# Kernel tuning notes

Measured on AMD Instinct MI355X. Metric: run time of the kernel, lower is better.

The kernel has to match this reference:

```python
import jax, jax.numpy as jnp
import numpy as np

N_NODES = 100000
N_EDGES = 1250000
D_IN = 32
H = 64
EPS = 1e-5


def layer_norm(x, g, b):
    mu = jnp.mean(x, axis=-1, keepdims=True)
    var = jnp.mean(jnp.square(x - mu), axis=-1, keepdims=True)
    return (x - mu) * jax.lax.rsqrt(var + EPS) * g + b


def setup_inputs() -> dict:
    key = jax.random.key(0)
    ks = jax.random.split(key, 6)
    x = jax.random.normal(ks[0], (N_NODES, D_IN), dtype=jnp.float32)
    edge_index = jax.random.randint(ks[1], (2, N_EDGES), 0, N_NODES, dtype=jnp.int64)
    W1 = jax.random.normal(ks[2], (D_IN, H), dtype=jnp.float32) * (1.0 / np.sqrt(D_IN))
    b1 = jax.random.normal(ks[3], (H,), dtype=jnp.float32) * 0.01
    W2 = jax.random.normal(ks[4], (H, H), dtype=jnp.float32) * (1.0 / np.sqrt(H))
    b2 = jax.random.normal(ks[5], (H,), dtype=jnp.float32) * 0.01
    g1 = jnp.ones((H,), dtype=jnp.float32)
    beta1 = jnp.zeros((H,), dtype=jnp.float32)
    g2 = jnp.ones((H,), dtype=jnp.float32)
    beta2 = jnp.zeros((H,), dtype=jnp.float32)
    return {"x": x, "edge_index": edge_index, "W1": W1, "b1": b1, "g1": g1,
            "beta1": beta1, "W2": W2, "b2": b2, "g2": g2, "beta2": beta2}


def reference(x, edge_index, W1, b1, g1, beta1, W2, b2, g2, beta2):
    # node MLP: Linear -> LN -> ReLU, twice
    h = jax.nn.relu(layer_norm(x @ W1 + b1, g1, beta1))
    h = jax.nn.relu(layer_norm(h @ W2 + b2, g2, beta2))
    # message passing: gather source features, scatter-add to destinations
    row, col = edge_index[0], edge_index[1]
    aggr = jax.ops.segment_sum(h[col], row, num_segments=N_NODES)  # [N, H]
    return h + aggr
```

## Files before the change

### kernel.cpp

```cpp
#include <hip/hip_runtime.h>

#define N_NODES 100000
#define D_IN 32
#define H 64
#define EPS 1e-5f
#define RSTR 32
#define CAP 32
#define OV_CAP 32768

typedef float floatx2 __attribute__((ext_vector_type(2)));

__device__ __forceinline__ unsigned short f2bf(float f) {
    union { float f; unsigned int u; } c; c.f = f;
    unsigned int b = c.u + 0x7FFFu + ((c.u >> 16) & 1u);
    return (unsigned short)(b >> 16);
}
__device__ __forceinline__ float bf2f(unsigned short s) {
    union { unsigned int u; float f; } c; c.u = ((unsigned int)s) << 16;
    return c.f;
}

__global__ __launch_bounds__(256, 2) void fused_kernel(
    const float* __restrict__ x,
    const float* __restrict__ W1, const float* __restrict__ b1,
    const float* __restrict__ g1, const float* __restrict__ be1,
    const float* __restrict__ W2, const float* __restrict__ b2,
    const float* __restrict__ g2, const float* __restrict__ be2,
    unsigned short* __restrict__ hb, unsigned char* __restrict__ hb8,
    const int* __restrict__ ei, int* __restrict__ cnt, int* __restrict__ bkt,
    int* __restrict__ ovCnt, int2* __restrict__ ov,
    int E, int SB, int TOT)
{
    const int i = blockIdx.x;
    const int before = (int)((long long)i * SB / TOT);
    const int after  = (int)((long long)(i + 1) * SB / TOT);

    if (after > before) {
        int t = before * 256 + threadIdx.x;
        int e0 = t * 8;
        if (e0 >= E) return;

        int rows[8], cols[8], pos[8];
        if (e0 + 7 < E) {
            int4 r0 = *(const int4*)(ei + e0);
            int4 r1 = *(const int4*)(ei + e0 + 4);
            int4 c0 = *(const int4*)(ei + E + e0);
            int4 c1 = *(const int4*)(ei + E + e0 + 4);
            rows[0]=r0.x; rows[1]=r0.y; rows[2]=r0.z; rows[3]=r0.w;
            rows[4]=r1.x; rows[5]=r1.y; rows[6]=r1.z; rows[7]=r1.w;
            cols[0]=c0.x; cols[1]=c0.y; cols[2]=c0.z; cols[3]=c0.w;
            cols[4]=c1.x; cols[5]=c1.y; cols[6]=c1.z; cols[7]=c1.w;
        } else {
#pragma unroll
            for (int j = 0; j < 8; ++j) {
                int e = e0 + j;
                if (e < E) { rows[j] = ei[e]; cols[j] = ei[E + e]; }
                else rows[j] = -1;
            }
        }
#pragma unroll
        for (int j = 0; j < 8; ++j)
            if (rows[j] >= 0) pos[j] = atomicAdd(&cnt[rows[j]], 1);
#pragma unroll
        for (int j = 0; j < 8; ++j) {
            if (rows[j] < 0) continue;
            if (pos[j] < CAP) {
                __builtin_nontemporal_store(cols[j], &bkt[rows[j] * RSTR + pos[j]]);
            } else {
                int s = atomicAdd(ovCnt, 1);
                if (s < OV_CAP) ov[s] = make_int2(rows[j], cols[j]);
            }
        }
        return;
    }

    int gid = (i - before) * 256 + threadIdx.x;
    int node = gid < N_NODES ? gid : N_NODES - 1;

    float xr[D_IN];
    {
        const float4* xp = (const float4*)(x + (long long)node * D_IN);
#pragma unroll
        for (int i2 = 0; i2 < D_IN / 4; ++i2) {
            float4 v = xp[i2];
            xr[4*i2+0] = v.x; xr[4*i2+1] = v.y; xr[4*i2+2] = v.z; xr[4*i2+3] = v.w;
        }
    }

    float h1[H];
#pragma unroll
    for (int jb = 0; jb < H / 4; ++jb) {
        float4 b = *(const float4*)(b1 + jb * 4);
        h1[4*jb+0] = b.x; h1[4*jb+1] = b.y; h1[4*jb+2] = b.z; h1[4*jb+3] = b.w;
    }
#pragma unroll
    for (int k = 0; k < D_IN; ++k) {
        float xk = xr[k];
#pragma unroll
        for (int jb = 0; jb < H / 4; ++jb) {
            float4 w = *(const float4*)(W1 + k * H + jb * 4);
            h1[4*jb+0] += xk * w.x; h1[4*jb+1] += xk * w.y;
            h1[4*jb+2] += xk * w.z; h1[4*jb+3] += xk * w.w;
        }
    }
    {
        float s0=0,s1=0,s2=0,s3=0, q0=0,q1=0,q2=0,q3=0;
#pragma unroll
        for (int j = 0; j < H; j += 4) {
            s0 += h1[j+0]; s1 += h1[j+1]; s2 += h1[j+2]; s3 += h1[j+3];
            q0 += h1[j+0]*h1[j+0]; q1 += h1[j+1]*h1[j+1];
            q2 += h1[j+2]*h1[j+2]; q3 += h1[j+3]*h1[j+3];
        }
        float mu  = (s0+s1+s2+s3) * (1.0f / H);
        float var = (q0+q1+q2+q3) * (1.0f / H) - mu * mu;
        float rs  = rsqrtf(var + EPS);
#pragma unroll
        for (int jb = 0; jb < H / 4; ++jb) {
            float4 g = *(const float4*)(g1 + jb * 4);
            float4 be = *(const float4*)(be1 + jb * 4);
            h1[4*jb+0] = fmaxf((h1[4*jb+0]-mu)*rs*g.x + be.x, 0.0f);
            h1[4*jb+1] = fmaxf((h1[4*jb+1]-mu)*rs*g.y + be.y, 0.0f);
            h1[4*jb+2] = fmaxf((h1[4*jb+2]-mu)*rs*g.z + be.z, 0.0f);
            h1[4*jb+3] = fmaxf((h1[4*jb+3]-mu)*rs*g.w + be.w, 0.0f);
        }
    }

    float h2[H];
#pragma unroll
    for (int jb = 0; jb < H / 4; ++jb) {
        float4 b = *(const float4*)(b2 + jb * 4);
        h2[4*jb+0] = b.x; h2[4*jb+1] = b.y; h2[4*jb+2] = b.z; h2[4*jb+3] = b.w;
    }
#pragma unroll
    for (int k = 0; k < H; ++k) {
        float hk = h1[k];
#pragma unroll
        for (int jb = 0; jb < H / 4; ++jb) {
            float4 w = *(const float4*)(W2 + k * H + jb * 4);
            h2[4*jb+0] += hk * w.x; h2[4*jb+1] += hk * w.y;
            h2[4*jb+2] += hk * w.z; h2[4*jb+3] += hk * w.w;
        }
    }
    {
        float s0=0,s1=0,s2=0,s3=0, q0=0,q1=0,q2=0,q3=0;
#pragma unroll
        for (int j = 0; j < H; j += 4) {
            s0 += h2[j+0]; s1 += h2[j+1]; s2 += h2[j+2]; s3 += h2[j+3];
            q0 += h2[j+0]*h2[j+0]; q1 += h2[j+1]*h2[j+1];
            q2 += h2[j+2]*h2[j+2]; q3 += h2[j+3]*h2[j+3];
        }
        float mu  = (s0+s1+s2+s3) * (1.0f / H);
        float var = (q0+q1+q2+q3) * (1.0f / H) - mu * mu;
        float rs  = rsqrtf(var + EPS);

        unsigned short* hp = hb + (long long)node * H;
        unsigned int w8[H / 4];
#pragma unroll
        for (int jb = 0; jb < H / 4; ++jb) {
            float4 g = *(const float4*)(g2 + jb * 4);
            float4 be = *(const float4*)(be2 + jb * 4);
            float4 v;
            v.x = fmaxf((h2[4*jb+0]-mu)*rs*g.x + be.x, 0.0f);
            v.y = fmaxf((h2[4*jb+1]-mu)*rs*g.y + be.y, 0.0f);
            v.z = fmaxf((h2[4*jb+2]-mu)*rs*g.z + be.z, 0.0f);
            v.w = fmaxf((h2[4*jb+3]-mu)*rs*g.w + be.w, 0.0f);
            ushort4 u;
            u.x = f2bf(v.x); u.y = f2bf(v.y); u.z = f2bf(v.z); u.w = f2bf(v.w);
            *(ushort4*)(hp + 4*jb) = u;
            int lo = __builtin_amdgcn_cvt_pk_fp8_f32(v.x, v.y, 0, false);
            w8[jb] = (unsigned int)__builtin_amdgcn_cvt_pk_fp8_f32(v.z, v.w, lo, true);
        }
        unsigned int* hp8 = (unsigned int*)(hb8 + (long long)node * H);
#pragma unroll
        for (int q = 0; q < H / 16; ++q)
            *(uint4*)(hp8 + q * 4) = make_uint4(w8[4*q+0], w8[4*q+1], w8[4*q+2], w8[4*q+3]);
    }
}

__global__ __launch_bounds__(256, 2) void aggr_kernel(
    const int* __restrict__ cnt, const int* __restrict__ bkt,
    const unsigned short* __restrict__ hb, const unsigned char* __restrict__ hb8,
    float* __restrict__ out,
    const int* __restrict__ ovCnt, const int2* __restrict__ ov)
{
    const int t    = threadIdx.x & 63;
    const int sub  = t >> 4;
    const int c    = t & 15;
    const int wave = blockIdx.x * 4 + (threadIdx.x >> 6);
    const int node = wave * 4 + sub;

    int m = cnt[node];
    if (m > CAP) m = CAP;
    const int base = node * RSTR;
    const unsigned int* h8 = (const unsigned int*)hb8;

    float a0 = 0.f, a1 = 0.f, a2 = 0.f, a3 = 0.f;
#pragma unroll
    for (int j0 = 0; j0 < CAP; j0 += 16) {
        int cc[16];
#pragma unroll
        for (int i = 0; i < 16; ++i)
            cc[i] = bkt[base + j0 + i];
        unsigned int vv[16];
#pragma unroll
        for (int i = 0; i < 16; ++i)
            if (j0 + i < m) vv[i] = h8[(cc[i] << 4) + c];
#pragma unroll
        for (int i = 0; i < 16; ++i) {
            if (j0 + i < m) {
                floatx2 p0 = __builtin_amdgcn_cvt_pk_f32_fp8(vv[i], false);
                floatx2 p1 = __builtin_amdgcn_cvt_pk_f32_fp8(vv[i], true);
                a0 += p0.x; a1 += p0.y; a2 += p1.x; a3 += p1.y;
            }
        }
    }

    {
        uint2 sv = *(const uint2*)(hb + ((long long)node << 6) + (c << 2));
        a0 += bf2f((unsigned short)(sv.x & 0xFFFFu));
        a1 += bf2f((unsigned short)(sv.x >> 16));
        a2 += bf2f((unsigned short)(sv.y & 0xFFFFu));
        a3 += bf2f((unsigned short)(sv.y >> 16));
    }

    int nov = *ovCnt; if (nov > OV_CAP) nov = OV_CAP;
    for (int i = 0; i < nov; ++i) {
        int2 rc = ov[i];
        if (rc.x == node) {
            uint2 vv = *(const uint2*)(hb + ((long long)rc.y << 6) + (c << 2));
            a0 += bf2f((unsigned short)(vv.x & 0xFFFFu));
            a1 += bf2f((unsigned short)(vv.x >> 16));
            a2 += bf2f((unsigned short)(vv.y & 0xFFFFu));
            a3 += bf2f((unsigned short)(vv.y >> 16));
        }
    }

    *(float4*)(out + ((long long)node << 6) + (c << 2)) = make_float4(a0, a1, a2, a3);
}

extern "C" void kernel_launch(void* const* d_in, const int* in_sizes, int n_in,
                              void* d_out, int out_size, void* d_ws, size_t ws_size,
                              hipStream_t stream)
{
    const float* x   = (const float*)d_in[0];
    const int*   ei  = (const int*)d_in[1];
    const float* W1  = (const float*)d_in[2];
    const float* b1  = (const float*)d_in[3];
    const float* g1  = (const float*)d_in[4];
    const float* be1 = (const float*)d_in[5];
    const float* W2  = (const float*)d_in[6];
    const float* b2  = (const float*)d_in[7];
    const float* g2  = (const float*)d_in[8];
    const float* be2 = (const float*)d_in[9];

    float* out = (float*)d_out;

    char* ws = (char*)d_ws;
    unsigned short* hb    = (unsigned short*)ws;
    unsigned char*  hb8   = (unsigned char*)(ws + 12800000);
    int*            cnt   = (int*)(ws + 19200000);
    int*            ovCnt = (int*)(ws + 19600000);
    int2*           ov    = (int2*)(ws + 19600064);
    int*            bkt   = (int*)(ws + 19862208);

    const int E = in_sizes[1] / 2;

    hipMemsetAsync(cnt, 0, 400064, stream);

    const int SB = ((E + 7) / 8 + 255) / 256;
    const int MB = (N_NODES + 255) / 256;
    fused_kernel<<<SB + MB, 256, 0, stream>>>(
        x, W1, b1, g1, be1, W2, b2, g2, be2, hb, hb8,
        ei, cnt, bkt, ovCnt, ov, E, SB, SB + MB);

    aggr_kernel<<<N_NODES / 16, 256, 0, stream>>>(cnt, bkt, hb, hb8, out, ovCnt, ov);
}
```

Before: 209.7 us.

## Partition edge buckets by source-node half and aggregate in two passes

Edges are bucketed per destination node into two sub-buckets of 16 slots, split by whether the gathered source node is in the lower or upper half of the node range. Aggregation then runs as two kernel launches, each gathering only from one half of the fp8 feature table, so each pass's working set is smaller and more likely to stay in cache. The second pass does a read-modify-write of the output. Per-half capacity drops to 16, which may push more edges into the overflow list that is scanned linearly. It also adds an extra launch and doubles the counter array and memset.

```diff
diff --git a/kernel.cpp b/kernel.cpp
--- a/kernel.cpp
+++ b/kernel.cpp
@@ -5,7 +5,8 @@
 #define H 64
 #define EPS 1e-5f
 #define RSTR 32
-#define CAP 32
+#define SCAP 16
+#define HALF 50000
 #define OV_CAP 32768
 
 typedef float floatx2 __attribute__((ext_vector_type(2)));
@@ -27,7 +28,7 @@
     const float* __restrict__ W2, const float* __restrict__ b2,
     const float* __restrict__ g2, const float* __restrict__ be2,
     unsigned short* __restrict__ hb, unsigned char* __restrict__ hb8,
-    const int* __restrict__ ei, int* __restrict__ cnt, int* __restrict__ bkt,
+    const int* __restrict__ ei, int* __restrict__ cnt2, int* __restrict__ bkt,
     int* __restrict__ ovCnt, int2* __restrict__ ov,
     int E, int SB, int TOT)
 {
@@ -40,7 +41,7 @@
         int e0 = t * 8;
         if (e0 >= E) return;
 
-        int rows[8], cols[8], pos[8];
+        int rows[8], cols[8], pos[8], gg[8];
         if (e0 + 7 < E) {
             int4 r0 = *(const int4*)(ei + e0);
             int4 r1 = *(const int4*)(ei + e0 + 4);
@@ -59,13 +60,18 @@
             }
         }
 #pragma unroll
-        for (int j = 0; j < 8; ++j)
-            if (rows[j] >= 0) pos[j] = atomicAdd(&cnt[rows[j]], 1);
+        for (int j = 0; j < 8; ++j) {
+            if (rows[j] >= 0) {
+                gg[j] = (cols[j] >= HALF) ? 1 : 0;
+                pos[j] = atomicAdd(&cnt2[rows[j] * 2 + gg[j]], 1);
+            }
+        }
 #pragma unroll
         for (int j = 0; j < 8; ++j) {
             if (rows[j] < 0) continue;
-            if (pos[j] < CAP) {
-                __builtin_nontemporal_store(cols[j], &bkt[rows[j] * RSTR + pos[j]]);
+            if (pos[j] < SCAP) {
+                __builtin_nontemporal_store(cols[j],
+                    &bkt[rows[j] * RSTR + gg[j] * SCAP + pos[j]]);
             } else {
                 int s = atomicAdd(ovCnt, 1);
                 if (s < OV_CAP) ov[s] = make_int2(rows[j], cols[j]);
@@ -177,11 +183,11 @@
     }
 }
 
-__global__ __launch_bounds__(256, 2) void aggr_kernel(
-    const int* __restrict__ cnt, const int* __restrict__ bkt,
+__global__ __launch_bounds__(256) void aggr_kernel(
+    const int* __restrict__ cnt2, const int* __restrict__ bkt,
     const unsigned short* __restrict__ hb, const unsigned char* __restrict__ hb8,
     float* __restrict__ out,
-    const int* __restrict__ ovCnt, const int2* __restrict__ ov)
+    const int* __restrict__ ovCnt, const int2* __restrict__ ov, int g)
 {
     const int t    = threadIdx.x & 63;
     const int sub  = t >> 4;
@@ -189,53 +195,52 @@
     const int wave = blockIdx.x * 4 + (threadIdx.x >> 6);
     const int node = wave * 4 + sub;
 
-    int m = cnt[node];
-    if (m > CAP) m = CAP;
-    const int base = node * RSTR;
+    int m = cnt2[node * 2 + g];
+    if (m > SCAP) m = SCAP;
+    const int base = node * RSTR + g * SCAP;
     const unsigned int* h8 = (const unsigned int*)hb8;
 
     float a0 = 0.f, a1 = 0.f, a2 = 0.f, a3 = 0.f;
-#pragma unroll
-    for (int j0 = 0; j0 < CAP; j0 += 16) {
-        int cc[16];
-#pragma unroll
-        for (int i = 0; i < 16; ++i)
-            cc[i] = bkt[base + j0 + i];
-        unsigned int vv[16];
-#pragma unroll
-        for (int i = 0; i < 16; ++i)
-            if (j0 + i < m) vv[i] = h8[(cc[i] << 4) + c];
-#pragma unroll
-        for (int i = 0; i < 16; ++i) {
-            if (j0 + i < m) {
-                floatx2 p0 = __builtin_amdgcn_cvt_pk_f32_fp8(vv[i], false);
-                floatx2 p1 = __builtin_amdgcn_cvt_pk_f32_fp8(vv[i], true);
-                a0 += p0.x; a1 += p0.y; a2 += p1.x; a3 += p1.y;
-            }
-        }
-    }
-
-    {
+    int cc[SCAP];
+#pragma unroll
+    for (int i = 0; i < SCAP; ++i)
+        cc[i] = bkt[base + i];
+    unsigned int vv[SCAP];
+#pragma unroll
+    for (int i = 0; i < SCAP; ++i)
+        if (i < m) vv[i] = h8[(cc[i] << 4) + c];
+#pragma unroll
+    for (int i = 0; i < SCAP; ++i) {
+        if (i < m) {
+            floatx2 p0 = __builtin_amdgcn_cvt_pk_f32_fp8(vv[i], false);
+            floatx2 p1 = __builtin_amdgcn_cvt_pk_f32_fp8(vv[i], true);
+            a0 += p0.x; a1 += p0.y; a2 += p1.x; a3 += p1.y;
+        }
+    }
+
+    float* op = out + ((long long)node << 6) + (c << 2);
+    if (g == 0) {
         uint2 sv = *(const uint2*)(hb + ((long long)node << 6) + (c << 2));
         a0 += bf2f((unsigned short)(sv.x & 0xFFFFu));
         a1 += bf2f((unsigned short)(sv.x >> 16));
         a2 += bf2f((unsigned short)(sv.y & 0xFFFFu));
         a3 += bf2f((unsigned short)(sv.y >> 16));
-    }
-
-    int nov = *ovCnt; if (nov > OV_CAP) nov = OV_CAP;
-    for (int i = 0; i < nov; ++i) {
-        int2 rc = ov[i];
-        if (rc.x == node) {
-            uint2 vv = *(const uint2*)(hb + ((long long)rc.y << 6) + (c << 2));
-            a0 += bf2f((unsigned short)(vv.x & 0xFFFFu));
-            a1 += bf2f((unsigned short)(vv.x >> 16));
-            a2 += bf2f((unsigned short)(vv.y & 0xFFFFu));
-            a3 += bf2f((unsigned short)(vv.y >> 16));
-        }
-    }
-
-    *(float4*)(out + ((long long)node << 6) + (c << 2)) = make_float4(a0, a1, a2, a3);
+        *(float4*)op = make_float4(a0, a1, a2, a3);
+    } else {
+        int nov = *ovCnt; if (nov > OV_CAP) nov = OV_CAP;
+        for (int i = 0; i < nov; ++i) {
+            int2 rc = ov[i];
+            if (rc.x == node) {
+                uint2 vb = *(const uint2*)(hb + ((long long)rc.y << 6) + (c << 2));
+                a0 += bf2f((unsigned short)(vb.x & 0xFFFFu));
+                a1 += bf2f((unsigned short)(vb.x >> 16));
+                a2 += bf2f((unsigned short)(vb.y & 0xFFFFu));
+                a3 += bf2f((unsigned short)(vb.y >> 16));
+            }
+        }
+        float4 prev = *(float4*)op;
+        *(float4*)op = make_float4(prev.x + a0, prev.y + a1, prev.z + a2, prev.w + a3);
+    }
 }
 
 extern "C" void kernel_launch(void* const* d_in, const int* in_sizes, int n_in,
@@ -258,20 +263,21 @@
     char* ws = (char*)d_ws;
     unsigned short* hb    = (unsigned short*)ws;
     unsigned char*  hb8   = (unsigned char*)(ws + 12800000);
-    int*            cnt   = (int*)(ws + 19200000);
-    int*            ovCnt = (int*)(ws + 19600000);
-    int2*           ov    = (int2*)(ws + 19600064);
-    int*            bkt   = (int*)(ws + 19862208);
+    int*            cnt2  = (int*)(ws + 19200000);
+    int*            ovCnt = (int*)(ws + 20000000);
+    int2*           ov    = (int2*)(ws + 20000064);
+    int*            bkt   = (int*)(ws + 20262208);
 
     const int E = in_sizes[1] / 2;
 
-    hipMemsetAsync(cnt, 0, 400064, stream);
+    hipMemsetAsync(cnt2, 0, 800064, stream);
 
     const int SB = ((E + 7) / 8 + 255) / 256;
     const int MB = (N_NODES + 255) / 256;
     fused_kernel<<<SB + MB, 256, 0, stream>>>(
         x, W1, b1, g1, be1, W2, b2, g2, be2, hb, hb8,
-        ei, cnt, bkt, ovCnt, ov, E, SB, SB + MB);
-
-    aggr_kernel<<<N_NODES / 16, 256, 0, stream>>>(cnt, bkt, hb, hb8, out, ovCnt, ov);
-}
+        ei, cnt2, bkt, ovCnt, ov, E, SB, SB + MB);
+
+    aggr_kernel<<<N_NODES / 16, 256, 0, stream>>>(cnt2, bkt, hb, hb8, out, ovCnt, ov, 0);
+    aggr_kernel<<<N_NODES / 16, 256, 0, stream>>>(cnt2, bkt, hb, hb8, out, ovCnt, ov, 1);
+}
```

After: 260.3 us. 1.24x slower.
